# Kernel tuning notes

Measured on AMD Instinct MI355X. Metric: run time of the kernel, lower is better.

The kernel has to match this reference:

```python
import jax, jax.numpy as jnp
import numpy as np

DIM = 192
D_STATE = 16
D_CONV = 4
EXPAND = 2
D_INNER = EXPAND * DIM
DT_RANK = -(-DIM // 16)  # ceil(dim/16) = 12


def setup_inputs() -> dict:
    key = jax.random.key(0)
    ks = jax.random.split(key, 9)
    B, T, H, W, C = 2, 16, 28, 28, DIM
    x = jax.random.normal(ks[0], (B, T, H, W, C), dtype=jnp.float32)
    s = lambda k, shp, fan: jax.random.normal(k, shp, dtype=jnp.float32) / np.sqrt(fan)
    params = {
        "norm_w": jnp.ones((DIM,), jnp.float32),
        "in_proj_w": s(ks[1], (DIM, 2 * D_INNER), DIM),
        "conv_w": s(ks[2], (D_INNER, D_CONV), D_CONV),
        "conv_b": jnp.zeros((D_INNER,), jnp.float32),
        "x_proj_w": s(ks[3], (D_INNER, DT_RANK + 2 * D_STATE), D_INNER),
        "dt_proj_w": s(ks[4], (DT_RANK, D_INNER), DT_RANK),
        "dt_proj_b": jnp.full((D_INNER,), float(np.log(np.expm1(0.01))), jnp.float32),
        "A_log": jnp.log(jnp.broadcast_to(jnp.arange(1, D_STATE + 1, dtype=jnp.float32), (D_INNER, D_STATE))),
        "D": jnp.ones((D_INNER,), jnp.float32),
        "out_proj_w": s(ks[5], (D_INNER, DIM), D_INNER),
    }
    return {"x": x, **params}


def _mamba_block(xs, norm_w, in_proj_w, conv_w, conv_b, x_proj_w,
                 dt_proj_w, dt_proj_b, A_log, D, out_proj_w):
    # xs: (N, T, C). Pre-RMSNorm + Mamba + residual.
    nrm = jax.lax.rsqrt(jnp.mean(xs * xs, axis=-1, keepdims=True) + 1e-6)
    xn = xs * nrm * norm_w

    xz = xn @ in_proj_w                      # (N, T, 2*Din)
    u, z = jnp.split(xz, 2, axis=-1)         # each (N, T, Din)

    # causal depthwise conv over T
    uc = jnp.transpose(u, (0, 2, 1))         # (N, Din, T)
    uc = jax.lax.conv_general_dilated(
        uc, conv_w[:, None, :], window_strides=(1,),
        padding=[(D_CONV - 1, 0)], feature_group_count=D_INNER)
    uc = jax.nn.silu(uc + conv_b[None, :, None])
    uc = jnp.transpose(uc, (0, 2, 1))        # (N, T, Din)

    dbl = uc @ x_proj_w                      # (N, T, dt_rank + 2*S)
    dt, Bm, Cm = jnp.split(dbl, [DT_RANK, DT_RANK + D_STATE], axis=-1)
    dt = jax.nn.softplus(dt @ dt_proj_w + dt_proj_b)   # (N, T, Din)
    A = -jnp.exp(A_log)                      # (Din, S)

    def step(h, inp):
        dt_t, B_t, C_t, u_t = inp            # (N,Din),(N,S),(N,S),(N,Din)
        dA = jnp.exp(dt_t[..., None] * A)    # (N, Din, S)
        h = h * dA + (dt_t * u_t)[..., None] * B_t[:, None, :]
        y = jnp.einsum('nds,ns->nd', h, C_t)
        return h, y

    N = uc.shape[0]
    h0 = jnp.zeros((N, D_INNER, D_STATE), dt.dtype)
    sw = lambda a: jnp.swapaxes(a, 0, 1)     # time-major for scan
    _, ys = jax.lax.scan(step, h0, (sw(dt), sw(Bm), sw(Cm), sw(uc)))
    y = jnp.swapaxes(ys, 0, 1) + uc * D      # (N, T, Din)
    y = y * jax.nn.silu(z)
    return xs + y @ out_proj_w


def reference(x, norm_w, in_proj_w, conv_w, conv_b, x_proj_w,
              dt_proj_w, dt_proj_b, A_log, D, out_proj_w):
    B, T, H, W, C = x.shape
    xs = jnp.transpose(x, (0, 2, 3, 1, 4)).reshape(B * H * W, T, C)
    out = _mamba_block(xs, norm_w, in_proj_w, conv_w, conv_b, x_proj_w,
                       dt_proj_w, dt_proj_b, A_log, D, out_proj_w)
    return jnp.transpose(out.reshape(B, H, W, T, C), (0, 3, 1, 2, 4))
```

## Files before the change

### kernel.cpp

```cpp
#include <hip/hip_runtime.h>

#define NSEQ 1568
#define TDIM 16
#define CDIM 192
#define DIN  384
#define SDIM 16
#define RNK  12
#define XZW  768
#define DBLW 44
#define HW784 784

#define XNP  200
#define DINP 392
#define DBLP 48

#define NT_IN 48
#define KT_IN 6
#define NT_OUT 12
#define KT_OUT 12
#define NT_XP 3
#define KT_XP 12
#define GRP_IN  (NT_IN*KT_IN*64)
#define GRP_OUT (NT_OUT*KT_OUT*64)
#define GRP_XP  (NT_XP*KT_XP*64)
#define OFF_OUT (GRP_IN*8)
#define OFF_XP  (OFF_OUT + GRP_OUT*8)
#define WS_NEED ((size_t)(OFF_XP + GRP_XP*8) * 2)

#define IN_EL  (CDIM*XZW)
#define OUT_EL (DIN*CDIM)
#define XP_EL  (GRP_XP*8)
#define PACK_TOT (IN_EL + OUT_EL + XP_EL)

typedef unsigned short u16;
typedef unsigned int   u32;
typedef __attribute__((ext_vector_type(8))) short short8;
typedef __attribute__((ext_vector_type(4))) float f32x4;

#define LOG2E 1.44269504f
#define LN2   0.69314718f

__device__ __forceinline__ float bf2f(u16 u) {
  union { u32 i; float f; } c; c.i = ((u32)u) << 16; return c.f;
}
__device__ __forceinline__ u16 f2bf(float f) {
  union { float f; u32 i; } c; c.f = f;
  u32 i = c.i;
  i += 0x7FFFu + ((i >> 16) & 1u);
  return (u16)(i >> 16);
}

__device__ __forceinline__ float ex2(float x) {
#if __has_builtin(__builtin_amdgcn_exp2f)
  return __builtin_amdgcn_exp2f(x);
#else
  return exp2f(x);
#endif
}
__device__ __forceinline__ float lg2(float x) {
#if __has_builtin(__builtin_amdgcn_logf)
  return __builtin_amdgcn_logf(x);
#else
  return log2f(x);
#endif
}
__device__ __forceinline__ float frcp(float x) {
#if __has_builtin(__builtin_amdgcn_rcpf)
  return __builtin_amdgcn_rcpf(x);
#else
  return 1.0f / x;
#endif
}
__device__ __forceinline__ float sigmoid_f(float s) {
  return frcp(1.0f + ex2(-LOG2E * s));
}
__device__ __forceinline__ float softplus_f(float a) {
  return fmaxf(a, 0.f) + LN2 * lg2(1.0f + ex2(-LOG2E * fabsf(a)));
}

template<bool B16>
__device__ __forceinline__ float ldg(const void* p, int i) {
  if (B16) return bf2f(((const u16*)p)[i]);
  return ((const float*)p)[i];
}
template<bool B16>
__device__ __forceinline__ void stg(void* p, int i, float v) {
  if (B16) ((u16*)p)[i] = f2bf(v);
  else     ((float*)p)[i] = v;
}

__device__ __forceinline__ bool probe_bf16(const void* x) {
  const u16* xu = (const u16*)x;
  int plaus = 0;
  #pragma unroll
  for (int k = 0; k < 32; ++k) {
    u16 v = xu[2*k];
    int e = (v >> 7) & 0xFF;
    plaus += ((e >= 100 && e <= 140) || v == 0) ? 1 : 0;
  }
  return plaus >= 16;
}

template<bool B16>
__device__ __forceinline__ void pack_body(const void* in_w, const void* out_w,
                                          const void* xp_w, u16* ws, int e) {
  if (e < IN_EL) {
    int k = e / XZW, n = e - k*XZW;
    int nt = n >> 4, l16 = n & 15, kt = k >> 5, q8 = (k & 31) >> 3, j = k & 7;
    int lane = q8*16 + l16;
    ws[((nt*KT_IN + kt)*64 + lane)*8 + j] = f2bf(ldg<B16>(in_w, e));
  } else if (e < IN_EL + OUT_EL) {
    int ee = e - IN_EL;
    int k = ee / CDIM, n = ee - k*CDIM;
    int nt = n >> 4, l16 = n & 15, kt = k >> 5, q8 = (k & 31) >> 3, j = k & 7;
    int lane = q8*16 + l16;
    ws[OFF_OUT + ((nt*KT_OUT + kt)*64 + lane)*8 + j] = f2bf(ldg<B16>(out_w, ee));
  } else if (e < PACK_TOT) {
    int ee = e - IN_EL - OUT_EL;
    int gg = ee >> 3, j = ee & 7;
    int lane = gg & 63, kt = (gg >> 6) % KT_XP, nt = gg / (64*KT_XP);
    int k = kt*32 + (lane >> 4)*8 + j, n = nt*16 + (lane & 15);
    ws[OFF_XP + ee] = f2bf(n < DBLW ? ldg<B16>(xp_w, k*DBLW + n) : 0.f);
  }
}

__global__ void pack_w(const void* __restrict__ x, const void* __restrict__ in_w,
                       const void* __restrict__ out_w, const void* __restrict__ xp_w,
                       u16* __restrict__ ws) {
  int e = blockIdx.x * blockDim.x + threadIdx.x;
  if (probe_bf16(x)) pack_body<true >(in_w, out_w, xp_w, ws, e);
  else               pack_body<false>(in_w, out_w, xp_w, ws, e);
}

struct Smem {
  float dbl[TDIM*DBLP];
  u16   xn [TDIM*XNP];
  u16   u  [TDIM*DINP];
  u16   z  [TDIM*DINP];
};

template<bool B16>
__device__ __forceinline__ void body(
    Smem& sm, const u16* __restrict__ ws,
    const void* __restrict__ x,        const void* __restrict__ norm_w,
    const void* __restrict__ conv_w,   const void* __restrict__ conv_b,
    const void* __restrict__ dt_proj_w,const void* __restrict__ dt_proj_b,
    const void* __restrict__ A_log,    const void* __restrict__ Dp,
    void* __restrict__ out)
{
  const int tid  = threadIdx.x;
  const int wid  = tid >> 6;
  const int lane = tid & 63;
  const int quad = lane >> 4;
  const int l16  = lane & 15;
  const int n  = blockIdx.x;
  const int b  = n / HW784;
  const int hw = n - b * HW784;

  {
    const int c0 = lane, c1 = lane + 64, c2 = lane + 128;
    float nw0 = ldg<B16>(norm_w, c0), nw1 = ldg<B16>(norm_w, c1), nw2 = ldg<B16>(norm_w, c2);
    for (int t = wid; t < TDIM; t += 6) {
      int base = ((b*TDIM + t)*HW784 + hw)*CDIM;
      float v0 = ldg<B16>(x, base + c0);
      float v1 = ldg<B16>(x, base + c1);
      float v2 = ldg<B16>(x, base + c2);
      float ss = v0*v0 + v1*v1 + v2*v2;
      #pragma unroll
      for (int off = 32; off > 0; off >>= 1) ss += __shfl_xor(ss, off, 64);
      float rs = rsqrtf(ss * (1.0f/CDIM) + 1e-6f);
      sm.xn[t*XNP + c0] = f2bf(v0 * rs * nw0);
      sm.xn[t*XNP + c1] = f2bf(v1 * rs * nw1);
      sm.xn[t*XNP + c2] = f2bf(v2 * rs * nw2);
    }
  }
  __syncthreads();

  {
    short8 afr[KT_IN];
    #pragma unroll
    for (int kt = 0; kt < KT_IN; ++kt)
      afr[kt] = *(const short8*)(sm.xn + l16*XNP + kt*32 + quad*8);
    #pragma unroll
    for (int g = 0; g < 2; ++g) {
      f32x4 acc[4];
      #pragma unroll
      for (int i = 0; i < 4; ++i) acc[i] = (f32x4)0.f;
      #pragma unroll
      for (int kt = 0; kt < KT_IN; ++kt) {
        #pragma unroll
        for (int i = 0; i < 4; ++i) {
          int ntg = wid*8 + g*4 + i;
          short8 bfr = *(const short8*)(ws + ((ntg*KT_IN + kt)*64 + lane)*8);
          acc[i] = __builtin_amdgcn_mfma_f32_16x16x32_bf16(afr[kt], bfr, acc[i], 0, 0, 0);
        }
      }
      #pragma unroll
      for (int i = 0; i < 4; ++i) {
        int ntg = wid*8 + g*4 + i;
        u16* dst = (ntg < 24) ? sm.u : sm.z;
        int col = ((ntg < 24) ? ntg*16 : (ntg-24)*16) + l16;
        #pragma unroll
        for (int r = 0; r < 4; ++r)
          dst[(quad*4 + r)*DINP + col] = f2bf(acc[i][r]);
      }
    }
  }
  __syncthreads();

  {
    const int d = tid;
    float w0 = ldg<B16>(conv_w, d*4+0), w1 = ldg<B16>(conv_w, d*4+1);
    float w2 = ldg<B16>(conv_w, d*4+2), w3 = ldg<B16>(conv_w, d*4+3);
    float bias = ldg<B16>(conv_b, d);
    float um1 = 0.f, um2 = 0.f, um3 = 0.f;
    #pragma unroll
    for (int t = 0; t < TDIM; ++t) {
      float cur = bf2f(sm.u[t*DINP + d]);
      float s = bias + cur*w3 + um1*w2 + um2*w1 + um3*w0;
      um3 = um2; um2 = um1; um1 = cur;
      sm.u[t*DINP + d] = f2bf(s * sigmoid_f(s));
    }
  }

  float wd[RNK];
  float dt_bias = ldg<B16>(dt_proj_b, tid);
  #pragma unroll
  for (int r = 0; r < RNK; ++r) wd[r] = ldg<B16>(dt_proj_w, r*DIN + tid);
  float Dv = ldg<B16>(Dp, tid);
  float a2;
  bool geo;
  {
    a2 = -LOG2E * ex2(LOG2E * ldg<B16>(A_log, tid*SDIM + 0));
    geo = true;
    #pragma unroll
    for (int s = 1; s < SDIM; ++s) {
      float as = -LOG2E * ex2(LOG2E * ldg<B16>(A_log, tid*SDIM + s));
      geo = geo && (fabsf(as - (float)(s+1)*a2) <= 1e-4f * fabsf(as) + 1e-30f);
    }
  }
  __syncthreads();

  if (wid < 3) {
    f32x4 acc = (f32x4)0.f;
    #pragma unroll
    for (int kt = 0; kt < KT_XP; ++kt) {
      short8 afr = *(const short8*)(sm.u + l16*DINP + kt*32 + quad*8);
      short8 bfr = *(const short8*)(ws + OFF_XP + ((wid*KT_XP + kt)*64 + lane)*8);
      acc = __builtin_amdgcn_mfma_f32_16x16x32_bf16(afr, bfr, acc, 0, 0, 0);
    }
    #pragma unroll
    for (int r = 0; r < 4; ++r)
      sm.dbl[(quad*4 + r)*DBLP + wid*16 + l16] = acc[r];
  }
  __syncthreads();

  {
    const int d = tid;
    float h[SDIM];
    #pragma unroll
    for (int s = 0; s < SDIM; ++s) h[s] = 0.f;
    if (geo) {
      for (int t = 0; t < TDIM; ++t) {
        const float* row = sm.dbl + t*DBLP;
        f32x4 d0 = *(const f32x4*)(row + 0);
        f32x4 d1 = *(const f32x4*)(row + 4);
        f32x4 d2 = *(const f32x4*)(row + 8);
        float a = dt_bias
          + d0[0]*wd[0] + d0[1]*wd[1] + d0[2]*wd[2]  + d0[3]*wd[3]
          + d1[0]*wd[4] + d1[1]*wd[5] + d1[2]*wd[6]  + d1[3]*wd[7]
          + d2[0]*wd[8] + d2[1]*wd[9] + d2[2]*wd[10] + d2[3]*wd[11];
        float dtv = softplus_f(a);
        float uv  = bf2f(sm.u[t*DINP + d]);
        float du  = dtv * uv;
        float q = ex2(dtv * a2);
        float Pq[SDIM];
        Pq[0] = q;        Pq[1] = q*q;       Pq[2] = Pq[1]*q;     Pq[3] = Pq[1]*Pq[1];
        Pq[4] = Pq[3]*q;  Pq[5] = Pq[3]*Pq[1]; Pq[6] = Pq[3]*Pq[2]; Pq[7] = Pq[3]*Pq[3];
        Pq[8] = Pq[7]*q;  Pq[9] = Pq[7]*Pq[1]; Pq[10]= Pq[7]*Pq[2]; Pq[11]= Pq[7]*Pq[3];
        Pq[12]= Pq[7]*Pq[4]; Pq[13]= Pq[7]*Pq[5]; Pq[14]= Pq[7]*Pq[6]; Pq[15]= Pq[7]*Pq[7];
        float y = 0.f;
        #pragma unroll
        for (int g = 0; g < 4; ++g) {
          f32x4 Bv = *(const f32x4*)(row + 12 + 4*g);
          f32x4 Cv = *(const f32x4*)(row + 28 + 4*g);
          #pragma unroll
          for (int j = 0; j < 4; ++j) {
            int s = 4*g + j;
            h[s] = h[s]*Pq[s] + du*Bv[j];
            y += h[s]*Cv[j];
          }
        }
        y += uv * Dv;
        float zv = bf2f(sm.z[t*DINP + d]);
        sm.z[t*DINP + d] = f2bf(y * (zv * sigmoid_f(zv)));
      }
    } else {
      float A2[SDIM];
      #pragma unroll
      for (int s = 0; s < SDIM; ++s)
        A2[s] = -LOG2E * ex2(LOG2E * ldg<B16>(A_log, d*SDIM + s));
      for (int t = 0; t < TDIM; ++t) {
        const float* row = sm.dbl + t*DBLP;
        f32x4 d0 = *(const f32x4*)(row + 0);
        f32x4 d1 = *(const f32x4*)(row + 4);
        f32x4 d2 = *(const f32x4*)(row + 8);
        float a = dt_bias
          + d0[0]*wd[0] + d0[1]*wd[1] + d0[2]*wd[2]  + d0[3]*wd[3]
          + d1[0]*wd[4] + d1[1]*wd[5] + d1[2]*wd[6]  + d1[3]*wd[7]
          + d2[0]*wd[8] + d2[1]*wd[9] + d2[2]*wd[10] + d2[3]*wd[11];
        float dtv = softplus_f(a);
        float uv  = bf2f(sm.u[t*DINP + d]);
        float du  = dtv * uv;
        float y = 0.f;
        #pragma unroll
        for (int g = 0; g < 4; ++g) {
          f32x4 Bv = *(const f32x4*)(row + 12 + 4*g);
          f32x4 Cv = *(const f32x4*)(row + 28 + 4*g);
          #pragma unroll
          for (int j = 0; j < 4; ++j) {
            int s = 4*g + j;
            float dA = ex2(dtv * A2[s]);
            h[s] = h[s]*dA + du*Bv[j];
            y += h[s]*Cv[j];
          }
        }
        y += uv * Dv;
        float zv = bf2f(sm.z[t*DINP + d]);
        sm.z[t*DINP + d] = f2bf(y * (zv * sigmoid_f(zv)));
      }
    }
  }
  __syncthreads();

  {
    f32x4 acc[2];
    acc[0] = (f32x4)0.f; acc[1] = (f32x4)0.f;
    #pragma unroll
    for (int kt = 0; kt < KT_OUT; ++kt) {
      short8 afr = *(const short8*)(sm.z + l16*DINP + kt*32 + quad*8);
      #pragma unroll
      for (int i = 0; i < 2; ++i) {
        int ntg = wid*2 + i;
        short8 bfr = *(const short8*)(ws + OFF_OUT + ((ntg*KT_OUT + kt)*64 + lane)*8);
        acc[i] = __builtin_amdgcn_mfma_f32_16x16x32_bf16(afr, bfr, acc[i], 0, 0, 0);
      }
    }
    #pragma unroll
    for (int i = 0; i < 2; ++i) {
      int col = (wid*2 + i)*16 + l16;
      #pragma unroll
      for (int r = 0; r < 4; ++r) {
        int row = quad*4 + r;
        int gi = ((b*TDIM + row)*HW784 + hw)*CDIM + col;
        float o = ldg<B16>(x, gi) + acc[i][r];
        stg<B16>(out, gi, o);
      }
    }
  }
}

__launch_bounds__(384, 6)
__global__ void mamba_mfma(
    const u16* __restrict__ ws,
    const void* __restrict__ x,        const void* __restrict__ norm_w,
    const void* __restrict__ conv_w,   const void* __restrict__ conv_b,
    const void* __restrict__ dt_proj_w,const void* __restrict__ dt_proj_b,
    const void* __restrict__ A_log,    const void* __restrict__ Dp,
    void* __restrict__ out)
{
  __shared__ Smem sm;
  if (probe_bf16(x))
    body<true >(sm, ws, x, norm_w, conv_w, conv_b, dt_proj_w, dt_proj_b, A_log, Dp, out);
  else
    body<false>(sm, ws, x, norm_w, conv_w, conv_b, dt_proj_w, dt_proj_b, A_log, Dp, out);
}

struct SmemF {
  float dt [TDIM*DIN];
  float dbl[TDIM*DBLW];
  u16   xs [TDIM*CDIM];
  u16   xn [TDIM*CDIM];
  u16   u  [TDIM*DIN];
  u16   z  [TDIM*DIN];
};

template<bool B16>
__device__ __forceinline__ void body_fb(
    SmemF& sm,
    const void* __restrict__ x,        const void* __restrict__ norm_w,
    const void* __restrict__ in_proj_w,const void* __restrict__ conv_w,
    const void* __restrict__ conv_b,   const void* __restrict__ x_proj_w,
    const void* __restrict__ dt_proj_w,const void* __restrict__ dt_proj_b,
    const void* __restrict__ A_log,    const void* __restrict__ Dp,
    const void* __restrict__ out_proj_w, void* __restrict__ out)
{
  const int tid = threadIdx.x;
  const int n  = blockIdx.x;
  const int b  = n / HW784;
  const int hw = n - b * HW784;

  for (int i = tid; i < TDIM*CDIM; i += 384) {
    int t = i / CDIM, c = i - t * CDIM;
    sm.xs[i] = f2bf(ldg<B16>(x, ((b*TDIM + t)*HW784 + hw)*CDIM + c));
  }
  __syncthreads();
  {
    int wave = tid >> 6, lane = tid & 63;
    for (int t = wave; t < TDIM; t += 6) {
      float ss = 0.f;
      for (int c = lane; c < CDIM; c += 64) {
        float v = bf2f(sm.xs[t*CDIM + c]); ss += v*v;
      }
      #pragma unroll
      for (int off = 32; off > 0; off >>= 1) ss += __shfl_xor(ss, off, 64);
      float rs = rsqrtf(ss * (1.0f/CDIM) + 1e-6f);
      for (int c = lane; c < CDIM; c += 64)
        sm.xn[t*CDIM + c] = f2bf(bf2f(sm.xs[t*CDIM + c]) * rs * ldg<B16>(norm_w, c));
    }
  }
  __syncthreads();
  {
    float acc0[TDIM], acc1[TDIM];
    #pragma unroll
    for (int t = 0; t < TDIM; ++t) { acc0[t] = 0.f; acc1[t] = 0.f; }
    const int j0 = 2 * tid;
    for (int c = 0; c < CDIM; c += 2) {
      float wA0 = ldg<B16>(in_proj_w,  c   *XZW + j0);
      float wA1 = ldg<B16>(in_proj_w,  c   *XZW + j0 + 1);
      float wB0 = ldg<B16>(in_proj_w, (c+1)*XZW + j0);
      float wB1 = ldg<B16>(in_proj_w, (c+1)*XZW + j0 + 1);
      #pragma unroll
      for (int t = 0; t < TDIM; ++t) {
        union { u32 i; float f; } c0, c1;
        u32 xv = *(const u32*)(sm.xn + t*CDIM + c);
        c0.i = xv << 16; c1.i = xv & 0xFFFF0000u;
        acc0[t] += c0.f*wA0 + c1.f*wB0;
        acc1[t] += c0.f*wA1 + c1.f*wB1;
      }
    }
    if (tid < 192) {
      #pragma unroll
      for (int t = 0; t < TDIM; ++t) {
        sm.u[t*DIN + j0]   = f2bf(acc0[t]);
        sm.u[t*DIN + j0+1] = f2bf(acc1[t]);
      }
    } else {
      int z0 = j0 - 384;
      #pragma unroll
      for (int t = 0; t < TDIM; ++t) {
        sm.z[t*DIN + z0]   = f2bf(acc0[t]);
        sm.z[t*DIN + z0+1] = f2bf(acc1[t]);
      }
    }
  }
  __syncthreads();
  {
    const int d = tid;
    float uv[TDIM];
    #pragma unroll
    for (int t = 0; t < TDIM; ++t) uv[t] = bf2f(sm.u[t*DIN + d]);
    float w0 = ldg<B16>(conv_w, d*4+0), w1 = ldg<B16>(conv_w, d*4+1);
    float w2 = ldg<B16>(conv_w, d*4+2), w3 = ldg<B16>(conv_w, d*4+3);
    float bias = ldg<B16>(conv_b, d);
    #pragma unroll
    for (int t = 0; t < TDIM; ++t) {
      float s = bias + uv[t]*w3;
      if (t >= 1) s += uv[t-1]*w2;
      if (t >= 2) s += uv[t-2]*w1;
      if (t >= 3) s += uv[t-3]*w0;
      float sg = 1.0f / (1.0f + __expf(-s));
      sm.u[t*DIN + d] = f2bf(s * sg);
    }
  }
  __syncthreads();
  for (int o = tid; o < TDIM*DBLW; o += 384) {
    int t = o / DBLW, j = o - t*DBLW;
    float acc = 0.f;
    for (int d = 0; d < DIN; ++d)
      acc += bf2f(sm.u[t*DIN + d]) * ldg<B16>(x_proj_w, d*DBLW + j);
    sm.dbl[o] = acc;
  }
  __syncthreads();
  {
    const int d = tid;
    float wd[RNK];
    #pragma unroll
    for (int r = 0; r < RNK; ++r) wd[r] = ldg<B16>(dt_proj_w, r*DIN + d);
    float bias = ldg<B16>(dt_proj_b, d);
    #pragma unroll
    for (int t = 0; t < TDIM; ++t) {
      float a = bias;
      #pragma unroll
      for (int r = 0; r < RNK; ++r) a += sm.dbl[t*DBLW + r] * wd[r];
      sm.dt[t*DIN + d] = fmaxf(a, 0.f) + log1pf(__expf(-fabsf(a)));
    }
  }
  __syncthreads();
  {
    const int d = tid;
    float A[SDIM], h[SDIM];
    #pragma unroll
    for (int s = 0; s < SDIM; ++s) {
      A[s] = -__expf(ldg<B16>(A_log, d*SDIM + s));
      h[s] = 0.f;
    }
    float Dv = ldg<B16>(Dp, d);
    for (int t = 0; t < TDIM; ++t) {
      float dtv = sm.dt[t*DIN + d];
      float uv  = bf2f(sm.u[t*DIN + d]);
      float du  = dtv * uv;
      float y = 0.f;
      #pragma unroll
      for (int s = 0; s < SDIM; ++s) {
        float dA = __expf(dtv * A[s]);
        h[s] = h[s]*dA + du * sm.dbl[t*DBLW + 12 + s];
        y += h[s] * sm.dbl[t*DBLW + 28 + s];
      }
      y += uv * Dv;
      float zv = bf2f(sm.z[t*DIN + d]);
      float sg = 1.0f / (1.0f + __expf(-zv));
      sm.dt[t*DIN + d] = y * (zv * sg);
    }
  }
  __syncthreads();
  {
    const int tt = tid / CDIM;
    const int c  = tid - tt*CDIM;
    float acc[8];
    #pragma unroll
    for (int i = 0; i < 8; ++i) acc[i] = 0.f;
    for (int d = 0; d < DIN; ++d) {
      float w = ldg<B16>(out_proj_w, d*CDIM + c);
      #pragma unroll
      for (int i = 0; i < 8; ++i)
        acc[i] += sm.dt[(tt*8 + i)*DIN + d] * w;
    }
    #pragma unroll
    for (int i = 0; i < 8; ++i) {
      int t = tt*8 + i;
      float o = bf2f(sm.xs[t*CDIM + c]) + acc[i];
      stg<B16>(out, ((b*TDIM + t)*HW784 + hw)*CDIM + c, o);
    }
  }
}

__launch_bounds__(384)
__global__ void mamba_fallback(
    const void* __restrict__ x,        const void* __restrict__ norm_w,
    const void* __restrict__ in_proj_w,const void* __restrict__ conv_w,
    const void* __restrict__ conv_b,   const void* __restrict__ x_proj_w,
    const void* __restrict__ dt_proj_w,const void* __restrict__ dt_proj_b,
    const void* __restrict__ A_log,    const void* __restrict__ Dp,
    const void* __restrict__ out_proj_w, void* __restrict__ out)
{
  __shared__ SmemF sm;
  if (probe_bf16(x))
    body_fb<true >(sm, x, norm_w, in_proj_w, conv_w, conv_b, x_proj_w,
                   dt_proj_w, dt_proj_b, A_log, Dp, out_proj_w, out);
  else
    body_fb<false>(sm, x, norm_w, in_proj_w, conv_w, conv_b, x_proj_w,
                   dt_proj_w, dt_proj_b, A_log, Dp, out_proj_w, out);
}

extern "C" void kernel_launch(void* const* d_in, const int* in_sizes, int n_in,
                              void* d_out, int out_size, void* d_ws, size_t ws_size,
                              hipStream_t stream) {
  if (ws_size >= WS_NEED) {
    pack_w<<<(PACK_TOT + 255) / 256, 256, 0, stream>>>(
        d_in[0], d_in[2], d_in[10], d_in[5], (u16*)d_ws);
    mamba_mfma<<<NSEQ, 384, 0, stream>>>(
        (const u16*)d_ws,
        d_in[0], d_in[1], d_in[3], d_in[4],
        d_in[6], d_in[7], d_in[8], d_in[9], d_out);
  } else {
    mamba_fallback<<<NSEQ, 384, 0, stream>>>(
        d_in[0], d_in[1], d_in[2], d_in[3], d_in[4], d_in[5],
        d_in[6], d_in[7], d_in[8], d_in[9], d_in[10], d_out);
  }
}
```

Measured before the change: 170.9 us.

## Transpose MFMA operands for vectorized stores and keep conv output in registers

Swaps the A/B operands of the MFMA calls so each lane holds four consecutive columns of one time step. The u/z, dbl and output-residual stores can then be packed vector writes, and the final residual add uses vector loads and stores. The conv output is also kept in registers for the scan, per-channel parameter loads are hoisted to kernel start, and packed weights now live in a static device global instead of the workspace. The non-MFMA fallback kernel is removed, and the non-geometric scan path now recomputes A from global memory inside its loop.

```diff
diff --git a/kernel.cpp b/kernel.cpp
--- a/kernel.cpp
+++ b/kernel.cpp
@@ -25,7 +25,7 @@
 #define GRP_XP  (NT_XP*KT_XP*64)
 #define OFF_OUT (GRP_IN*8)
 #define OFF_XP  (OFF_OUT + GRP_OUT*8)
-#define WS_NEED ((size_t)(OFF_XP + GRP_XP*8) * 2)
+#define WS_ELEMS (OFF_XP + GRP_XP*8)
 
 #define IN_EL  (CDIM*XZW)
 #define OUT_EL (DIN*CDIM)
@@ -36,9 +36,12 @@
 typedef unsigned int   u32;
 typedef __attribute__((ext_vector_type(8))) short short8;
 typedef __attribute__((ext_vector_type(4))) float f32x4;
+typedef __attribute__((ext_vector_type(2))) unsigned int u32x2;
 
 #define LOG2E 1.44269504f
 #define LN2   0.69314718f
+
+__device__ __align__(16) u16 g_ws[WS_ELEMS];
 
 __device__ __forceinline__ float bf2f(u16 u) {
   union { u32 i; float f; } c; c.i = ((u32)u) << 16; return c.f;
@@ -84,9 +87,27 @@
   return ((const float*)p)[i];
 }
 template<bool B16>
-__device__ __forceinline__ void stg(void* p, int i, float v) {
-  if (B16) ((u16*)p)[i] = f2bf(v);
-  else     ((float*)p)[i] = v;
+__device__ __forceinline__ f32x4 ld4(const void* p, int i) {
+  f32x4 r;
+  if (B16) {
+    u32x2 raw = *(const u32x2*)((const u16*)p + i);
+    r[0] = bf2f((u16)(raw[0] & 0xFFFF)); r[1] = bf2f((u16)(raw[0] >> 16));
+    r[2] = bf2f((u16)(raw[1] & 0xFFFF)); r[3] = bf2f((u16)(raw[1] >> 16));
+  } else {
+    r = *(const f32x4*)((const float*)p + i);
+  }
+  return r;
+}
+template<bool B16>
+__device__ __forceinline__ void st4(void* p, int i, f32x4 v) {
+  if (B16) {
+    u32x2 o;
+    o[0] = ((u32)f2bf(v[1]) << 16) | f2bf(v[0]);
+    o[1] = ((u32)f2bf(v[3]) << 16) | f2bf(v[2]);
+    *(u32x2*)((u16*)p + i) = o;
+  } else {
+    *(f32x4*)((float*)p + i) = v;
+  }
 }
 
 __device__ __forceinline__ bool probe_bf16(const void* x) {
@@ -103,33 +124,34 @@
 
 template<bool B16>
 __device__ __forceinline__ void pack_body(const void* in_w, const void* out_w,
-                                          const void* xp_w, u16* ws, int e) {
+                                          const void* xp_w, int e) {
   if (e < IN_EL) {
     int k = e / XZW, n = e - k*XZW;
     int nt = n >> 4, l16 = n & 15, kt = k >> 5, q8 = (k & 31) >> 3, j = k & 7;
     int lane = q8*16 + l16;
-    ws[((nt*KT_IN + kt)*64 + lane)*8 + j] = f2bf(ldg<B16>(in_w, e));
+    g_ws[((nt*KT_IN + kt)*64 + lane)*8 + j] = f2bf(ldg<B16>(in_w, e));
   } else if (e < IN_EL + OUT_EL) {
     int ee = e - IN_EL;
     int k = ee / CDIM, n = ee - k*CDIM;
     int nt = n >> 4, l16 = n & 15, kt = k >> 5, q8 = (k & 31) >> 3, j = k & 7;
     int lane = q8*16 + l16;
-    ws[OFF_OUT + ((nt*KT_OUT + kt)*64 + lane)*8 + j] = f2bf(ldg<B16>(out_w, ee));
+    g_ws[OFF_OUT + ((nt*KT_OUT + kt)*64 + lane)*8 + j] = f2bf(ldg<B16>(out_w, ee));
   } else if (e < PACK_TOT) {
     int ee = e - IN_EL - OUT_EL;
     int gg = ee >> 3, j = ee & 7;
     int lane = gg & 63, kt = (gg >> 6) % KT_XP, nt = gg / (64*KT_XP);
     int k = kt*32 + (lane >> 4)*8 + j, n = nt*16 + (lane & 15);
-    ws[OFF_XP + ee] = f2bf(n < DBLW ? ldg<B16>(xp_w, k*DBLW + n) : 0.f);
+    g_ws[OFF_XP + ee] = f2bf(n < DBLW ? ldg<B16>(xp_w, k*DBLW + n) : 0.f);
   }
 }
 
 __global__ void pack_w(const void* __restrict__ x, const void* __restrict__ in_w,
-                       const void* __restrict__ out_w, const void* __restrict__ xp_w,
-                       u16* __restrict__ ws) {
+                       const void* __restrict__ out_w, const void* __restrict__ xp_w) {
   int e = blockIdx.x * blockDim.x + threadIdx.x;
-  if (probe_bf16(x)) pack_body<true >(in_w, out_w, xp_w, ws, e);
-  else               pack_body<false>(in_w, out_w, xp_w, ws, e);
+  if (e < PACK_TOT) {
+    if (probe_bf16(x)) pack_body<true >(in_w, out_w, xp_w, e);
+    else               pack_body<false>(in_w, out_w, xp_w, e);
+  }
 }
 
 struct Smem {
@@ -141,7 +163,7 @@
 
 template<bool B16>
 __device__ __forceinline__ void body(
-    Smem& sm, const u16* __restrict__ ws,
+    Smem& sm,
     const void* __restrict__ x,        const void* __restrict__ norm_w,
     const void* __restrict__ conv_w,   const void* __restrict__ conv_b,
     const void* __restrict__ dt_proj_w,const void* __restrict__ dt_proj_b,
@@ -153,9 +175,26 @@
   const int lane = tid & 63;
   const int quad = lane >> 4;
   const int l16  = lane & 15;
+  const u16* ws = g_ws;
   const int n  = blockIdx.x;
   const int b  = n / HW784;
   const int hw = n - b * HW784;
+
+  float cw0 = ldg<B16>(conv_w, tid*4+0), cw1 = ldg<B16>(conv_w, tid*4+1);
+  float cw2 = ldg<B16>(conv_w, tid*4+2), cw3 = ldg<B16>(conv_w, tid*4+3);
+  float cbias = ldg<B16>(conv_b, tid);
+  float wd[RNK];
+  float dt_bias = ldg<B16>(dt_proj_b, tid);
+  #pragma unroll
+  for (int r = 0; r < RNK; ++r) wd[r] = ldg<B16>(dt_proj_w, r*DIN + tid);
+  float Dv = ldg<B16>(Dp, tid);
+  float a2 = -LOG2E * ex2(LOG2E * ldg<B16>(A_log, tid*SDIM + 0));
+  bool geo = true;
+  #pragma unroll
+  for (int s = 1; s < SDIM; ++s) {
+    float as = -LOG2E * ex2(LOG2E * ldg<B16>(A_log, tid*SDIM + s));
+    geo = geo && (fabsf(as - (float)(s+1)*a2) <= 1e-4f * fabsf(as) + 1e-30f);
+  }
 
   {
     const int c0 = lane, c1 = lane + 64, c2 = lane + 128;
@@ -177,10 +216,10 @@
   __syncthreads();
 
   {
-    short8 afr[KT_IN];
+    short8 xfr[KT_IN];
     #pragma unroll
     for (int kt = 0; kt < KT_IN; ++kt)
-      afr[kt] = *(const short8*)(sm.xn + l16*XNP + kt*32 + quad*8);
+      xfr[kt] = *(const short8*)(sm.xn + l16*XNP + kt*32 + quad*8);
     #pragma unroll
     for (int g = 0; g < 2; ++g) {
       f32x4 acc[4];
@@ -191,52 +230,36 @@
         #pragma unroll
         for (int i = 0; i < 4; ++i) {
           int ntg = wid*8 + g*4 + i;
-          short8 bfr = *(const short8*)(ws + ((ntg*KT_IN + kt)*64 + lane)*8);
-          acc[i] = __builtin_amdgcn_mfma_f32_16x16x32_bf16(afr[kt], bfr, acc[i], 0, 0, 0);
+          short8 wfr = *(const short8*)(ws + ((ntg*KT_IN + kt)*64 + lane)*8);
+          acc[i] = __builtin_amdgcn_mfma_f32_16x16x32_bf16(wfr, xfr[kt], acc[i], 0, 0, 0);
         }
       }
       #pragma unroll
       for (int i = 0; i < 4; ++i) {
         int ntg = wid*8 + g*4 + i;
-        u16* dst = (ntg < 24) ? sm.u : sm.z;
-        int col = ((ntg < 24) ? ntg*16 : (ntg-24)*16) + l16;
-        #pragma unroll
-        for (int r = 0; r < 4; ++r)
-          dst[(quad*4 + r)*DINP + col] = f2bf(acc[i][r]);
-      }
-    }
-  }
-  __syncthreads();
-
+        u16* dst  = (ntg < 24) ? sm.u : sm.z;
+        int col0  = ((ntg < 24) ? ntg*16 : (ntg-24)*16) + quad*4;
+        u32x2 o;
+        o[0] = ((u32)f2bf(acc[i][1]) << 16) | f2bf(acc[i][0]);
+        o[1] = ((u32)f2bf(acc[i][3]) << 16) | f2bf(acc[i][2]);
+        *(u32x2*)(dst + l16*DINP + col0) = o;
+      }
+    }
+  }
+  __syncthreads();
+
+  float uvr[TDIM];
   {
     const int d = tid;
-    float w0 = ldg<B16>(conv_w, d*4+0), w1 = ldg<B16>(conv_w, d*4+1);
-    float w2 = ldg<B16>(conv_w, d*4+2), w3 = ldg<B16>(conv_w, d*4+3);
-    float bias = ldg<B16>(conv_b, d);
     float um1 = 0.f, um2 = 0.f, um3 = 0.f;
     #pragma unroll
     for (int t = 0; t < TDIM; ++t) {
       float cur = bf2f(sm.u[t*DINP + d]);
-      float s = bias + cur*w3 + um1*w2 + um2*w1 + um3*w0;
+      float s = cbias + cur*cw3 + um1*cw2 + um2*cw1 + um3*cw0;
       um3 = um2; um2 = um1; um1 = cur;
-      sm.u[t*DINP + d] = f2bf(s * sigmoid_f(s));
-    }
-  }
-
-  float wd[RNK];
-  float dt_bias = ldg<B16>(dt_proj_b, tid);
-  #pragma unroll
-  for (int r = 0; r < RNK; ++r) wd[r] = ldg<B16>(dt_proj_w, r*DIN + tid);
-  float Dv = ldg<B16>(Dp, tid);
-  float a2;
-  bool geo;
-  {
-    a2 = -LOG2E * ex2(LOG2E * ldg<B16>(A_log, tid*SDIM + 0));
-    geo = true;
-    #pragma unroll
-    for (int s = 1; s < SDIM; ++s) {
-      float as = -LOG2E * ex2(LOG2E * ldg<B16>(A_log, tid*SDIM + s));
-      geo = geo && (fabsf(as - (float)(s+1)*a2) <= 1e-4f * fabsf(as) + 1e-30f);
+      float v = s * sigmoid_f(s);
+      uvr[t] = v;
+      sm.u[t*DINP + d] = f2bf(v);
     }
   }
   __syncthreads();
@@ -245,13 +268,11 @@
     f32x4 acc = (f32x4)0.f;
     #pragma unroll
     for (int kt = 0; kt < KT_XP; ++kt) {
-      short8 afr = *(const short8*)(sm.u + l16*DINP + kt*32 + quad*8);
-      short8 bfr = *(const short8*)(ws + OFF_XP + ((wid*KT_XP + kt)*64 + lane)*8);
-      acc = __builtin_amdgcn_mfma_f32_16x16x32_bf16(afr, bfr, acc, 0, 0, 0);
-    }
-    #pragma unroll
-    for (int r = 0; r < 4; ++r)
-      sm.dbl[(quad*4 + r)*DBLP + wid*16 + l16] = acc[r];
+      short8 ufr = *(const short8*)(sm.u + l16*DINP + kt*32 + quad*8);
+      short8 wfr = *(const short8*)(ws + OFF_XP + ((wid*KT_XP + kt)*64 + lane)*8);
+      acc = __builtin_amdgcn_mfma_f32_16x16x32_bf16(wfr, ufr, acc, 0, 0, 0);
+    }
+    *(f32x4*)(sm.dbl + l16*DBLP + wid*16 + quad*4) = acc;
   }
   __syncthreads();
 
@@ -271,11 +292,11 @@
           + d1[0]*wd[4] + d1[1]*wd[5] + d1[2]*wd[6]  + d1[3]*wd[7]
           + d2[0]*wd[8] + d2[1]*wd[9] + d2[2]*wd[10] + d2[3]*wd[11];
         float dtv = softplus_f(a);
-        float uv  = bf2f(sm.u[t*DINP + d]);
+        float uv  = uvr[t];
         float du  = dtv * uv;
         float q = ex2(dtv * a2);
         float Pq[SDIM];
-        Pq[0] = q;        Pq[1] = q*q;       Pq[2] = Pq[1]*q;     Pq[3] = Pq[1]*Pq[1];
+        Pq[0] = q;        Pq[1] = q*q;         Pq[2] = Pq[1]*q;     Pq[3] = Pq[1]*Pq[1];
         Pq[4] = Pq[3]*q;  Pq[5] = Pq[3]*Pq[1]; Pq[6] = Pq[3]*Pq[2]; Pq[7] = Pq[3]*Pq[3];
         Pq[8] = Pq[7]*q;  Pq[9] = Pq[7]*Pq[1]; Pq[10]= Pq[7]*Pq[2]; Pq[11]= Pq[7]*Pq[3];
         Pq[12]= Pq[7]*Pq[4]; Pq[13]= Pq[7]*Pq[5]; Pq[14]= Pq[7]*Pq[6]; Pq[15]= Pq[7]*Pq[7];
@@ -296,34 +317,21 @@
         sm.z[t*DINP + d] = f2bf(y * (zv * sigmoid_f(zv)));
       }
     } else {
-      float A2[SDIM];
-      #pragma unroll
-      for (int s = 0; s < SDIM; ++s)
-        A2[s] = -LOG2E * ex2(LOG2E * ldg<B16>(A_log, d*SDIM + s));
       for (int t = 0; t < TDIM; ++t) {
         const float* row = sm.dbl + t*DBLP;
-        f32x4 d0 = *(const f32x4*)(row + 0);
-        f32x4 d1 = *(const f32x4*)(row + 4);
-        f32x4 d2 = *(const f32x4*)(row + 8);
-        float a = dt_bias
-          + d0[0]*wd[0] + d0[1]*wd[1] + d0[2]*wd[2]  + d0[3]*wd[3]
-          + d1[0]*wd[4] + d1[1]*wd[5] + d1[2]*wd[6]  + d1[3]*wd[7]
-          + d2[0]*wd[8] + d2[1]*wd[9] + d2[2]*wd[10] + d2[3]*wd[11];
+        float a = dt_bias;
+        #pragma unroll
+        for (int r = 0; r < RNK; ++r) a += row[r] * wd[r];
         float dtv = softplus_f(a);
-        float uv  = bf2f(sm.u[t*DINP + d]);
+        float uv  = uvr[t];
         float du  = dtv * uv;
         float y = 0.f;
         #pragma unroll
-        for (int g = 0; g < 4; ++g) {
-          f32x4 Bv = *(const f32x4*)(row + 12 + 4*g);
-          f32x4 Cv = *(const f32x4*)(row + 28 + 4*g);
-          #pragma unroll
-          for (int j = 0; j < 4; ++j) {
-            int s = 4*g + j;
-            float dA = ex2(dtv * A2[s]);
-            h[s] = h[s]*dA + du*Bv[j];
-            y += h[s]*Cv[j];
-          }
+        for (int s = 0; s < SDIM; ++s) {
+          float As = -LOG2E * ex2(LOG2E * ldg<B16>(A_log, d*SDIM + s));
+          float dA = ex2(dtv * As);
+          h[s] = h[s]*dA + du * row[12 + s];
+          y += h[s] * row[28 + s];
         }
         y += uv * Dv;
         float zv = bf2f(sm.z[t*DINP + d]);
@@ -338,244 +346,49 @@
     acc[0] = (f32x4)0.f; acc[1] = (f32x4)0.f;
     #pragma unroll
     for (int kt = 0; kt < KT_OUT; ++kt) {
-      short8 afr = *(const short8*)(sm.z + l16*DINP + kt*32 + quad*8);
+      short8 yfr = *(const short8*)(sm.z + l16*DINP + kt*32 + quad*8);
       #pragma unroll
       for (int i = 0; i < 2; ++i) {
         int ntg = wid*2 + i;
-        short8 bfr = *(const short8*)(ws + OFF_OUT + ((ntg*KT_OUT + kt)*64 + lane)*8);
-        acc[i] = __builtin_amdgcn_mfma_f32_16x16x32_bf16(afr, bfr, acc[i], 0, 0, 0);
+        short8 wfr = *(const short8*)(ws + OFF_OUT + ((ntg*KT_OUT + kt)*64 + lane)*8);
+        acc[i] = __builtin_amdgcn_mfma_f32_16x16x32_bf16(wfr, yfr, acc[i], 0, 0, 0);
       }
     }
     #pragma unroll
     for (int i = 0; i < 2; ++i) {
-      int col = (wid*2 + i)*16 + l16;
-      #pragma unroll
-      for (int r = 0; r < 4; ++r) {
-        int row = quad*4 + r;
-        int gi = ((b*TDIM + row)*HW784 + hw)*CDIM + col;
-        float o = ldg<B16>(x, gi) + acc[i][r];
-        stg<B16>(out, gi, o);
-      }
+      int c0 = (wid*2 + i)*16 + quad*4;
+      int t  = l16;
+      int gi = ((b*TDIM + t)*HW784 + hw)*CDIM + c0;
+      f32x4 xv = ld4<B16>(x, gi);
+      f32x4 o;
+      #pragma unroll
+      for (int r = 0; r < 4; ++r) o[r] = xv[r] + acc[i][r];
+      st4<B16>(out, gi, o);
     }
   }
 }
 
 __launch_bounds__(384, 6)
 __global__ void mamba_mfma(
-    const u16* __restrict__ ws,
     const void* __restrict__ x,        const void* __restrict__ norm_w,
     const void* __restrict__ conv_w,   const void* __restrict__ conv_b,
-    const void* __restrict__ dt_proj_w,const void* __restrict__ dt_proj_b,
+    const void* __restrict__ dt_w,     const void* __restrict__ dt_b,
     const void* __restrict__ A_log,    const void* __restrict__ Dp,
     void* __restrict__ out)
 {
   __shared__ Smem sm;
   if (probe_bf16(x))
-    body<true >(sm, ws, x, norm_w, conv_w, conv_b, dt_proj_w, dt_proj_b, A_log, Dp, out);
+    body<true >(sm, x, norm_w, conv_w, conv_b, dt_w, dt_b, A_log, Dp, out);
   else
-    body<false>(sm, ws, x, norm_w, conv_w, conv_b, dt_proj_w, dt_proj_b, A_log, Dp, out);
-}
-
-struct SmemF {
-  float dt [TDIM*DIN];
-  float dbl[TDIM*DBLW];
-  u16   xs [TDIM*CDIM];
-  u16   xn [TDIM*CDIM];
-  u16   u  [TDIM*DIN];
-  u16   z  [TDIM*DIN];
-};
-
-template<bool B16>
-__device__ __forceinline__ void body_fb(
-    SmemF& sm,
-    const void* __restrict__ x,        const void* __restrict__ norm_w,
-    const void* __restrict__ in_proj_w,const void* __restrict__ conv_w,
-    const void* __restrict__ conv_b,   const void* __restrict__ x_proj_w,
-    const void* __restrict__ dt_proj_w,const void* __restrict__ dt_proj_b,
-    const void* __restrict__ A_log,    const void* __restrict__ Dp,
-    const void* __restrict__ out_proj_w, void* __restrict__ out)
-{
-  const int tid = threadIdx.x;
-  const int n  = blockIdx.x;
-  const int b  = n / HW784;
-  const int hw = n - b * HW784;
-
-  for (int i = tid; i < TDIM*CDIM; i += 384) {
-    int t = i / CDIM, c = i - t * CDIM;
-    sm.xs[i] = f2bf(ldg<B16>(x, ((b*TDIM + t)*HW784 + hw)*CDIM + c));
-  }
-  __syncthreads();
-  {
-    int wave = tid >> 6, lane = tid & 63;
-    for (int t = wave; t < TDIM; t += 6) {
-      float ss = 0.f;
-      for (int c = lane; c < CDIM; c += 64) {
-        float v = bf2f(sm.xs[t*CDIM + c]); ss += v*v;
-      }
-      #pragma unroll
-      for (int off = 32; off > 0; off >>= 1) ss += __shfl_xor(ss, off, 64);
-      float rs = rsqrtf(ss * (1.0f/CDIM) + 1e-6f);
-      for (int c = lane; c < CDIM; c += 64)
-        sm.xn[t*CDIM + c] = f2bf(bf2f(sm.xs[t*CDIM + c]) * rs * ldg<B16>(norm_w, c));
-    }
-  }
-  __syncthreads();
-  {
-    float acc0[TDIM], acc1[TDIM];
-    #pragma unroll
-    for (int t = 0; t < TDIM; ++t) { acc0[t] = 0.f; acc1[t] = 0.f; }
-    const int j0 = 2 * tid;
-    for (int c = 0; c < CDIM; c += 2) {
-      float wA0 = ldg<B16>(in_proj_w,  c   *XZW + j0);
-      float wA1 = ldg<B16>(in_proj_w,  c   *XZW + j0 + 1);
-      float wB0 = ldg<B16>(in_proj_w, (c+1)*XZW + j0);
-      float wB1 = ldg<B16>(in_proj_w, (c+1)*XZW + j0 + 1);
-      #pragma unroll
-      for (int t = 0; t < TDIM; ++t) {
-        union { u32 i; float f; } c0, c1;
-        u32 xv = *(const u32*)(sm.xn + t*CDIM + c);
-        c0.i = xv << 16; c1.i = xv & 0xFFFF0000u;
-        acc0[t] += c0.f*wA0 + c1.f*wB0;
-        acc1[t] += c0.f*wA1 + c1.f*wB1;
-      }
-    }
-    if (tid < 192) {
-      #pragma unroll
-      for (int t = 0; t < TDIM; ++t) {
-        sm.u[t*DIN + j0]   = f2bf(acc0[t]);
-        sm.u[t*DIN + j0+1] = f2bf(acc1[t]);
-      }
-    } else {
-      int z0 = j0 - 384;
-      #pragma unroll
-      for (int t = 0; t < TDIM; ++t) {
-        sm.z[t*DIN + z0]   = f2bf(acc0[t]);
-        sm.z[t*DIN + z0+1] = f2bf(acc1[t]);
-      }
-    }
-  }
-  __syncthreads();
-  {
-    const int d = tid;
-    float uv[TDIM];
-    #pragma unroll
-    for (int t = 0; t < TDIM; ++t) uv[t] = bf2f(sm.u[t*DIN + d]);
-    float w0 = ldg<B16>(conv_w, d*4+0), w1 = ldg<B16>(conv_w, d*4+1);
-    float w2 = ldg<B16>(conv_w, d*4+2), w3 = ldg<B16>(conv_w, d*4+3);
-    float bias = ldg<B16>(conv_b, d);
-    #pragma unroll
-    for (int t = 0; t < TDIM; ++t) {
-      float s = bias + uv[t]*w3;
-      if (t >= 1) s += uv[t-1]*w2;
-      if (t >= 2) s += uv[t-2]*w1;
-      if (t >= 3) s += uv[t-3]*w0;
-      float sg = 1.0f / (1.0f + __expf(-s));
-      sm.u[t*DIN + d] = f2bf(s * sg);
-    }
-  }
-  __syncthreads();
-  for (int o = tid; o < TDIM*DBLW; o += 384) {
-    int t = o / DBLW, j = o - t*DBLW;
-    float acc = 0.f;
-    for (int d = 0; d < DIN; ++d)
-      acc += bf2f(sm.u[t*DIN + d]) * ldg<B16>(x_proj_w, d*DBLW + j);
-    sm.dbl[o] = acc;
-  }
-  __syncthreads();
-  {
-    const int d = tid;
-    float wd[RNK];
-    #pragma unroll
-    for (int r = 0; r < RNK; ++r) wd[r] = ldg<B16>(dt_proj_w, r*DIN + d);
-    float bias = ldg<B16>(dt_proj_b, d);
-    #pragma unroll
-    for (int t = 0; t < TDIM; ++t) {
-      float a = bias;
-      #pragma unroll
-      for (int r = 0; r < RNK; ++r) a += sm.dbl[t*DBLW + r] * wd[r];
-      sm.dt[t*DIN + d] = fmaxf(a, 0.f) + log1pf(__expf(-fabsf(a)));
-    }
-  }
-  __syncthreads();
-  {
-    const int d = tid;
-    float A[SDIM], h[SDIM];
-    #pragma unroll
-    for (int s = 0; s < SDIM; ++s) {
-      A[s] = -__expf(ldg<B16>(A_log, d*SDIM + s));
-      h[s] = 0.f;
-    }
-    float Dv = ldg<B16>(Dp, d);
-    for (int t = 0; t < TDIM; ++t) {
-      float dtv = sm.dt[t*DIN + d];
-      float uv  = bf2f(sm.u[t*DIN + d]);
-      float du  = dtv * uv;
-      float y = 0.f;
-      #pragma unroll
-      for (int s = 0; s < SDIM; ++s) {
-        float dA = __expf(dtv * A[s]);
-        h[s] = h[s]*dA + du * sm.dbl[t*DBLW + 12 + s];
-        y += h[s] * sm.dbl[t*DBLW + 28 + s];
-      }
-      y += uv * Dv;
-      float zv = bf2f(sm.z[t*DIN + d]);
-      float sg = 1.0f / (1.0f + __expf(-zv));
-      sm.dt[t*DIN + d] = y * (zv * sg);
-    }
-  }
-  __syncthreads();
-  {
-    const int tt = tid / CDIM;
-    const int c  = tid - tt*CDIM;
-    float acc[8];
-    #pragma unroll
-    for (int i = 0; i < 8; ++i) acc[i] = 0.f;
-    for (int d = 0; d < DIN; ++d) {
-      float w = ldg<B16>(out_proj_w, d*CDIM + c);
-      #pragma unroll
-      for (int i = 0; i < 8; ++i)
-        acc[i] += sm.dt[(tt*8 + i)*DIN + d] * w;
-    }
-    #pragma unroll
-    for (int i = 0; i < 8; ++i) {
-      int t = tt*8 + i;
-      float o = bf2f(sm.xs[t*CDIM + c]) + acc[i];
-      stg<B16>(out, ((b*TDIM + t)*HW784 + hw)*CDIM + c, o);
-    }
-  }
-}
-
-__launch_bounds__(384)
-__global__ void mamba_fallback(
-    const void* __restrict__ x,        const void* __restrict__ norm_w,
-    const void* __restrict__ in_proj_w,const void* __restrict__ conv_w,
-    const void* __restrict__ conv_b,   const void* __restrict__ x_proj_w,
-    const void* __restrict__ dt_proj_w,const void* __restrict__ dt_proj_b,
-    const void* __restrict__ A_log,    const void* __restrict__ Dp,
-    const void* __restrict__ out_proj_w, void* __restrict__ out)
-{
-  __shared__ SmemF sm;
-  if (probe_bf16(x))
-    body_fb<true >(sm, x, norm_w, in_proj_w, conv_w, conv_b, x_proj_w,
-                   dt_proj_w, dt_proj_b, A_log, Dp, out_proj_w, out);
-  else
-    body_fb<false>(sm, x, norm_w, in_proj_w, conv_w, conv_b, x_proj_w,
-                   dt_proj_w, dt_proj_b, A_log, Dp, out_proj_w, out);
+    body<false>(sm, x, norm_w, conv_w, conv_b, dt_w, dt_b, A_log, Dp, out);
 }
 
 extern "C" void kernel_launch(void* const* d_in, const int* in_sizes, int n_in,
                               void* d_out, int out_size, void* d_ws, size_t ws_size,
                               hipStream_t stream) {
-  if (ws_size >= WS_NEED) {
-    pack_w<<<(PACK_TOT + 255) / 256, 256, 0, stream>>>(
-        d_in[0], d_in[2], d_in[10], d_in[5], (u16*)d_ws);
-    mamba_mfma<<<NSEQ, 384, 0, stream>>>(
-        (const u16*)d_ws,
-        d_in[0], d_in[1], d_in[3], d_in[4],
-        d_in[6], d_in[7], d_in[8], d_in[9], d_out);
-  } else {
-    mamba_fallback<<<NSEQ, 384, 0, stream>>>(
-        d_in[0], d_in[1], d_in[2], d_in[3], d_in[4], d_in[5],
-        d_in[6], d_in[7], d_in[8], d_in[9], d_in[10], d_out);
-  }
-}
+  pack_w<<<(PACK_TOT + 255) / 256, 256, 0, stream>>>(
+      d_in[0], d_in[2], d_in[10], d_in[5]);
+  mamba_mfma<<<NSEQ, 384, 0, stream>>>(
+      d_in[0], d_in[1], d_in[3], d_in[4],
+      d_in[6], d_in[7], d_in[8], d_in[9], d_out);
+}
```

Result: slower. 206.6 us (+20.9%).
